# Kernel tuning notes

Measured on AMD Instinct MI355X. Metric: run time of the kernel, lower is better.

Reference implementation:

```python
import jax, jax.numpy as jnp
import numpy as np

DIMS = [1536, 2048, 2560, 3072, 1792, 2304, 2816, 2048, 2560, 3328]

def _ln(x, g, b, eps=1e-5):
    m = jnp.mean(x, -1, keepdims=True)
    v = jnp.mean((x - m) ** 2, -1, keepdims=True)
    return (x - m) / jnp.sqrt(v + eps) * g + b

def _gelu(x):
    return jax.nn.gelu(x, approximate=False)

def _mish(x):
    return x * jnp.tanh(jax.nn.softplus(x))

_ACTS = [jax.nn.silu, _gelu, _mish, jax.nn.relu, jax.nn.selu, jnp.tanh, jax.nn.softplus, jax.nn.elu]

def _renorm_sparse_topk(probs, active_k, max_k):
    vals, idx = jax.lax.top_k(probs, max_k)
    mask = (jnp.arange(max_k)[None, :] < active_k[:, None]).astype(probs.dtype)
    n = probs.shape[0]
    sparse = jnp.zeros_like(probs).at[jnp.arange(n)[:, None], idx].set(vals * mask)
    return sparse / jnp.clip(jnp.sum(sparse, -1, keepdims=True), 1e-6, None)

def setup_inputs():
    N, IN, OUT, E, M, S, SUB, DST, INNER, SH = 2048, 1024, 10, 10, 24, 4, 4, 40, 768, 2048
    DMAX = max(DIMS)
    ks = iter(jax.random.split(jax.random.key(0), 80))
    def p(shape, std=0.02):
        return jax.random.normal(next(ks), shape, jnp.float32) * std
    eu = np.zeros((E, DMAX, IN), np.float32)
    ed = np.zeros((E, OUT, DMAX), np.float32)
    for i in range(E):
        d = DIMS[i % len(DIMS)]
        eu[i, :d] = np.asarray(p((d, IN), 0.02))
        ed[i, :, :d] = np.asarray(p((OUT, d), 0.01))
    return {
        'x': jax.random.normal(next(ks), (N, IN), jnp.float32),
        'weight': p((OUT, IN), 0.03), 'bias': p((OUT,), 0.01),
        'shared_up_w': p((SH, IN)), 'shared_down_w': p((OUT, SH), 0.01),
        'shared_norm_g': jnp.ones((OUT,)), 'shared_norm_b': jnp.zeros((OUT,)),
        'shared_scale': jnp.asarray(1.0, jnp.float32),
        'memory_keys': p((M, IN)), 'memory_values_init': p((M, IN)),
        'memory_query_w': p((IN, IN), 0.01), 'memory_out_w': p((OUT, IN), 0.01),
        'mem_wgate_w': p((M, 2 * IN), 0.01), 'mem_wgate_b': jnp.zeros((M,)),
        'mem_wval_w': p((IN, IN), 0.01), 'mem_wval_b': jnp.zeros((IN,)),
        'depth_q_w': p((IN, IN), 0.01), 'depth_k_w': p((IN, IN), 0.01),
        'depth_v_w': p((IN, IN), 0.01), 'depth_out_w': p((OUT, IN), 0.01),
        'cell_ln_g': jnp.ones((S, IN)), 'cell_ln_b': jnp.zeros((S, IN)),
        'cell_fc1_w': p((S, INNER, IN)), 'cell_fc1_b': jnp.zeros((S, INNER)),
        'cell_fc2_w': p((S, IN, INNER)), 'cell_fc2_b': jnp.zeros((S, IN)),
        'ssm_a_w': p((DST, IN), 0.01), 'ssm_a_b': jnp.zeros((DST,)),
        'ssm_b_w': p((IN, DST), 0.01), 'ssm_b_b': jnp.zeros((IN,)),
        'mor_sub_w': p((SUB, E, IN)), 'mor_sub_b': jnp.zeros((SUB, E)),
        'mor_mix_w': p((SUB, IN)), 'mor_mix_b': jnp.zeros((SUB,)),
        'expert_bias': jnp.zeros((E,)),
        'budget_w': p((4, IN)), 'budget_b': jnp.zeros((4,)),
        'experts_up': jnp.asarray(eu), 'experts_down': jnp.asarray(ed),
        'expert_norm_g': jnp.ones((E, OUT)), 'expert_norm_b': jnp.zeros((E, OUT)),
        'halt_w': p((S, 1, IN), 0.01), 'halt_b': jnp.full((S, 1), -2.0, jnp.float32),
        'alpha': jnp.asarray(0.1, jnp.float32), 'beta': jnp.asarray(0.1, jnp.float32),
    }

def reference(x, weight, bias, shared_up_w, shared_down_w, shared_norm_g, shared_norm_b, shared_scale, memory_keys, memory_values_init, memory_query_w, memory_out_w, mem_wgate_w, mem_wgate_b, mem_wval_w, mem_wval_b, depth_q_w, depth_k_w, depth_v_w, depth_out_w, cell_ln_g, cell_ln_b, cell_fc1_w, cell_fc1_b, cell_fc2_w, cell_fc2_b, ssm_a_w, ssm_a_b, ssm_b_w, ssm_b_b, mor_sub_w, mor_sub_b, mor_mix_w, mor_mix_b, expert_bias, budget_w, budget_b, experts_up, experts_down, expert_norm_g, expert_norm_b, halt_w, halt_b, alpha, beta):
    in_dim = x.shape[-1]
    x_flat = x.reshape(-1, in_dim)
    n = x_flat.shape[0]
    base = x_flat @ weight.T + bias
    shared = _ln(jax.nn.silu(x_flat @ shared_up_w.T) @ shared_down_w.T, shared_norm_g, shared_norm_b)
    mem_vals = jnp.broadcast_to(memory_values_init[None], (n,) + memory_values_init.shape)
    current = x_flat
    total = jnp.zeros_like(base)
    cum_halt = jnp.zeros((n, 1), x.dtype)
    bank = []
    mem_scale = in_dim ** -0.5
    steps = cell_ln_g.shape[0]
    n_exp = expert_bias.shape[0]
    max_topk = min(4, n_exp)
    for step in range(steps):
        mq = current @ memory_query_w.T
        mem_attn = jax.nn.softmax((mq @ memory_keys.T) * mem_scale, -1)  # [n, M]
        mem_ctx = jnp.einsum('nm,nmd->nd', mem_attn, mem_vals)
        if bank:
            ds = jnp.stack(bank, 1)  # [n, s, d]
            q = current @ depth_q_w.T
            k = ds @ depth_k_w.T
            v = ds @ depth_v_w.T
            attn = jax.nn.softmax(jnp.einsum('nd,nsd->ns', q, k) * mem_scale, -1)
            depth_ctx = jnp.einsum('ns,nsd->nd', attn, v)
        else:
            depth_ctx = jnp.zeros_like(current)
        ssm_corr = jnp.tanh(current @ ssm_a_w.T + ssm_a_b) @ ssm_b_w.T + ssm_b_b
        enriched = current + 0.34 * mem_ctx + 0.22 * depth_ctx + 0.18 * ssm_corr
        h = _gelu(_ln(enriched, cell_ln_g[step], cell_ln_b[step]) @ cell_fc1_w[step].T + cell_fc1_b[step])
        current = enriched + h @ cell_fc2_w[step].T + cell_fc2_b[step]
        bank.append(current)
        sub = jnp.einsum('nd,sed->nse', current, mor_sub_w) + mor_sub_b[None]
        mix = jax.nn.softmax(current @ mor_mix_w.T + mor_mix_b, -1)
        gate_probs = jax.nn.softmax(jnp.einsum('ns,nse->ne', mix, sub) + expert_bias, -1)
        budget = 1 + jnp.argmax(jax.nn.softmax(current @ budget_w.T + budget_b, -1), -1)
        sg = _renorm_sparse_topk(gate_probs, budget, max_topk)
        expert_logits = jnp.zeros_like(base)
        for i in range(n_exp):
            d = DIMS[i % len(DIMS)]
            hh = _ACTS[i % len(_ACTS)](current @ experts_up[i, :d, :].T)
            eo = _ln(hh @ experts_down[i, :, :d].T, expert_norm_g[i], expert_norm_b[i])
            expert_logits = expert_logits + sg[:, i:i + 1] * eo
        step_logits = expert_logits + 0.22 * (mem_ctx @ memory_out_w.T) + 0.14 * (depth_ctx @ depth_out_w.T)
        surprise = 1.0 - jnp.max(sg, -1, keepdims=True)  # [n, 1]
        wg = jax.nn.softmax(jnp.concatenate([current, mem_ctx], -1) @ mem_wgate_w.T + mem_wgate_b, -1)
        wv = (current @ mem_wval_w.T + mem_wval_b)[:, None, :]
        mem_vals = mem_vals + surprise[..., None] * wg[..., None] * (wv - mem_vals)
        halt = jax.nn.sigmoid((current + 0.2 * mem_ctx + 0.1 * depth_ctx) @ halt_w[step].T + halt_b[step])
        remaining = 1.0 - cum_halt
        total = total + remaining * step_logits
        cum_halt = cum_halt + remaining * halt
    total = total / float(steps)
    out = base + shared_scale * shared + (alpha + 1e-4) * total + beta * (current @ memory_out_w.T)
    return out.reshape(x.shape[:-1] + (out.shape[-1],))
```

## Files before the change

kernel.cpp:

```cpp
#include <hip/hip_runtime.h>
#include <stdint.h>

#define N_TOK 2048
#define IN_D  1024
#define NEXP  10
#define NSTEP 4
#define INNER 768
#define SHD   2048
#define DMAX  3328
#define DSUM  24064

typedef __attribute__((ext_vector_type(4))) float f32x4;
typedef __attribute__((ext_vector_type(8))) short bf16x8;

__device__ const int c_dims[10] = {1536,2048,2560,3072,1792,2304,2816,2048,2560,3328};
__device__ const int c_offs[10] = {0,1536,3584,6144,9216,11008,13312,16128,18176,20736};
__device__ const int c_acts[10] = {0,1,2,3,4,5,6,7,0,1};
__device__ const int c_cum[11]  = {0,12,28,48,72,86,104,126,142,162,188};

__device__ __forceinline__ float wred(float v){
#pragma unroll
  for (int s = 32; s > 0; s >>= 1) v += __shfl_xor(v, s, 64);
  return v;
}
__device__ __forceinline__ float wmax(float v){
#pragma unroll
  for (int s = 32; s > 0; s >>= 1) v = fmaxf(v, __shfl_xor(v, s, 64));
  return v;
}
__device__ __forceinline__ float bf2f(uint16_t u){
  return __uint_as_float(((uint32_t)u) << 16);
}
__device__ __forceinline__ uint16_t f2bf(float f){
  uint32_t u = __float_as_uint(f);
  return (uint16_t)((u + 0x7FFFu + ((u >> 16) & 1u)) >> 16);
}
__device__ __forceinline__ uint8_t f2fp8(float f){
  uint32_t u = __float_as_uint(f);
  uint8_t sign = (uint8_t)((u >> 24) & 0x80u);
  uint32_t absu = u & 0x7FFFFFFFu;
  if (absu >= 0x43E00000u) return sign | 0x7Eu;
  if (absu < 0x3C800000u){
    float af = __uint_as_float(absu);
    int q = (int)rintf(af * 512.0f);
    return sign | (uint8_t)q;
  }
  uint32_t mant = absu & 0x7FFFFFu;
  uint32_t exp = absu >> 23;
  uint32_t lsb = (mant >> 20) & 1u;
  uint32_t rounded = mant + 0x7FFFFu + lsb;
  if (rounded >= 0x800000u){ exp += 1; rounded = 0; }
  uint32_t e8 = exp - 120;
  uint32_t m8 = (rounded >> 20) & 7u;
  if (e8 > 15u || (e8 == 15u && m8 == 7u)) return sign | 0x7Eu;
  return sign | (uint8_t)((e8 << 3) | m8);
}
__device__ __forceinline__ void gload16(const uint16_t* g, uint16_t* l){
  __builtin_amdgcn_global_load_lds(
      (const __attribute__((address_space(1))) uint32_t*)(const void*)g,
      (__attribute__((address_space(3))) uint32_t*)(void*)l, 16, 0, 0);
}
__device__ __forceinline__ void gload16b(const void* g, void* l){
  __builtin_amdgcn_global_load_lds(
      (const __attribute__((address_space(1))) uint32_t*)g,
      (__attribute__((address_space(3))) uint32_t*)l, 16, 0, 0);
}

__device__ __forceinline__ float actf(int a, float x){
  switch(a){
    case 0: return x / (1.f + expf(-x));
    case 1: return 0.5f * x * (1.f + erff(x * 0.7071067811865475f));
    case 2: { float sp = fmaxf(x,0.f) + log1pf(expf(-fabsf(x)));
              return x * tanhf(sp); }
    case 3: return fmaxf(x, 0.f);
    case 4: return x > 0.f ? 1.0507009873554805f * x
                           : 1.7580993408473768f * expm1f(x);
    case 5: return tanhf(x);
    case 6: return fmaxf(x,0.f) + log1pf(expf(-fabsf(x)));
    default: return x > 0.f ? x : expm1f(x);
  }
}

__global__ void split_kernel(const float* __restrict__ src, uint16_t* __restrict__ hi,
                             uint16_t* __restrict__ lo, size_t n){
  size_t i = ((size_t)blockIdx.x * blockDim.x + threadIdx.x) << 2;
  size_t stride = ((size_t)gridDim.x * blockDim.x) << 2;
  for (; i < n; i += stride){
    float4 v = *(const float4*)(src + i);
    ushort4 h, l;
    h.x = f2bf(v.x); l.x = f2bf(v.x - bf2f(h.x));
    h.y = f2bf(v.y); l.y = f2bf(v.y - bf2f(h.y));
    h.z = f2bf(v.z); l.z = f2bf(v.z - bf2f(h.z));
    h.w = f2bf(v.w); l.w = f2bf(v.w - bf2f(h.w));
    *(ushort4*)(hi + i) = h;
    *(ushort4*)(lo + i) = l;
  }
}
__global__ void split_strided(const float* __restrict__ src, uint16_t* __restrict__ hi,
                              uint16_t* __restrict__ lo, int rows, int cols, int ldd){
  int nq = rows * (cols >> 2);
  for (int i = blockIdx.x * blockDim.x + threadIdx.x; i < nq; i += gridDim.x * blockDim.x){
    int r = i / (cols >> 2), c4 = (i - r * (cols >> 2)) << 2;
    float4 v = *(const float4*)(src + (size_t)r * cols + c4);
    ushort4 h, l;
    h.x = f2bf(v.x); l.x = f2bf(v.x - bf2f(h.x));
    h.y = f2bf(v.y); l.y = f2bf(v.y - bf2f(h.y));
    h.z = f2bf(v.z); l.z = f2bf(v.z - bf2f(h.z));
    h.w = f2bf(v.w); l.w = f2bf(v.w - bf2f(h.w));
    size_t d = (size_t)r * ldd + c4;
    *(ushort4*)(hi + d) = h;
    *(ushort4*)(lo + d) = l;
  }
}
__global__ void cvt_fp8_kernel(const float* __restrict__ src, uint8_t* __restrict__ dst, size_t n){
  size_t i = ((size_t)blockIdx.x * blockDim.x + threadIdx.x) << 2;
  size_t stride = ((size_t)gridDim.x * blockDim.x) << 2;
  for (; i < n; i += stride){
    float4 v = *(const float4*)(src + i);
    uchar4 q;
    q.x = f2fp8(v.x); q.y = f2fp8(v.y); q.z = f2fp8(v.z); q.w = f2fp8(v.w);
    *(uchar4*)(dst + i) = q;
  }
}
__global__ void fill1_kernel(float* __restrict__ p, int n){
  int i = blockIdx.x * blockDim.x + threadIdx.x;
  if (i < n) p[i] = 1.f;
}
__global__ void tr_sbw_kernel(const float* __restrict__ src, float* __restrict__ dst){
  int i = blockIdx.x * 256 + threadIdx.x;
  if (i < 40 * 1024){
    int o = i >> 10, d = i & 1023;
    dst[i] = src[d * 40 + o];
  }
}

__global__ __launch_bounds__(256)
void k2_kernel(const float* __restrict__ keys, const float* __restrict__ mqw,
               float* __restrict__ K2){
  int m = blockIdx.x;
  int j = blockIdx.y * 256 + threadIdx.x;
  float acc = 0.f;
  for (int d = 0; d < 1024; d++)
    acc = fmaf(keys[m * 1024 + d], mqw[d * 1024 + j], acc);
  K2[m * 1024 + j] = acc;
}

__global__ void build_routew(const float* __restrict__ msw, const float* __restrict__ mmw,
                             const float* __restrict__ bw, const float* __restrict__ wgw,
                             const float* __restrict__ hw, const float* __restrict__ mow,
                             const float* __restrict__ dow, uint16_t* __restrict__ Wh,
                             uint16_t* __restrict__ Wl){
  const int TOT = 4 * 128 * 3072;
  for (int i = blockIdx.x * 256 + threadIdx.x; i < TOT; i += gridDim.x * 256){
    int t = i / (128 * 3072);
    int rem = i - t * (128 * 3072);
    int row = rem / 3072, col = rem - row * 3072;
    float v = 0.f;
    if (row < 40){ if (col < 1024) v = msw[row * 1024 + col]; }
    else if (row < 44){ if (col < 1024) v = mmw[(row - 40) * 1024 + col]; }
    else if (row < 48){ if (col < 1024) v = bw[(row - 44) * 1024 + col]; }
    else if (row < 72){ if (col < 2048) v = wgw[(row - 48) * 2048 + col]; }
    else if (row == 72){
      if (col < 1024) v = hw[t * 1024 + col];
      else if (col < 2048) v = 0.2f * hw[t * 1024 + col - 1024];
      else v = 0.1f * hw[t * 1024 + col - 2048];
    }
    else if (row < 83){ if (col >= 1024 && col < 2048) v = mow[(row - 73) * 1024 + col - 1024]; }
    else if (row < 93){ if (col >= 2048) v = dow[(row - 83) * 1024 + col - 2048]; }
    else if (row < 103){ if (col < 1024) v = mow[(row - 93) * 1024 + col]; }
    uint16_t h = f2bf(v);
    Wh[i] = h; Wl[i] = f2bf(v - bf2f(h));
  }
}

enum { EPI_GELU=0, EPI_CUR=1, EPI_PRE=2, EPI_QROUTE=3 };

template<int EPI>
__global__ __launch_bounds__(256)
void gemm_sp(const uint16_t* __restrict__ Ah, const uint16_t* __restrict__ Al, int lda,
             const uint16_t* __restrict__ Wh, const uint16_t* __restrict__ Wl,
             const uint16_t* __restrict__ W2h, const uint16_t* __restrict__ W2l,
             const float* __restrict__ bias, const float* __restrict__ addend,
             float* __restrict__ D0, float* __restrict__ D1, float* __restrict__ D2,
             float* __restrict__ D3, uint8_t* __restrict__ o8,
             uint16_t* __restrict__ oH, uint16_t* __restrict__ oL,
             int K, int D)
{
  __shared__ __align__(16) uint16_t sm[4][2][4096];
  int tid = threadIdx.x, lane = tid & 63, wave = tid >> 6;
  int wr = wave >> 1, wc = wave & 1;
  int arow = lane & 15, agrp = lane >> 4;
  int rowBase = blockIdx.y * 128;
  bool isRoute = (EPI == EPI_QROUTE) && ((int)blockIdx.x < 4);
  const uint16_t* Wsh = isRoute ? W2h : Wh;
  const uint16_t* Wsl = isRoute ? W2l : Wl;
  int wst     = isRoute ? 3072 : K;
  int colBase = isRoute ? 0 : ((EPI == EPI_QROUTE ? (int)blockIdx.x - 4 : (int)blockIdx.x) * 128);
  int kBase   = isRoute ? (int)blockIdx.x * 768 : 0;
  int kLen    = isRoute ? 768 : K;
  f32x4 acc[4][4];
#pragma unroll
  for (int m = 0; m < 4; m++)
#pragma unroll
    for (int n = 0; n < 4; n++){ f32x4 z = {0.f,0.f,0.f,0.f}; acc[m][n] = z; }

#define STAGE_G(buf, k0) do { \
  _Pragma("unroll") \
  for (int s = 0; s < 2; s++){ \
    int u = tid + s * 256; \
    int rr = u >> 2; \
    int ch = (u & 3) ^ ((rr >> 1) & 3); \
    size_t ga = (size_t)(rowBase + rr) * lda + kBase + (k0) + ch * 8; \
    size_t gw = (size_t)(colBase + rr) * wst + kBase + (k0) + ch * 8; \
    gload16(&Ah[ga], &sm[0][buf][u << 3]); \
    gload16(&Al[ga], &sm[1][buf][u << 3]); \
    gload16(&Wsh[gw], &sm[2][buf][u << 3]); \
    gload16(&Wsl[gw], &sm[3][buf][u << 3]); \
  } } while(0)

  int nk = kLen >> 5;
  STAGE_G(0, 0);
  if (nk > 1) STAGE_G(1, 32);
  int perm = (arow >> 1) & 3;
#pragma unroll 1
  for (int ki = 0; ki < nk; ki++){
    int cb = ki & 1;
    if (ki + 1 < nk) asm volatile("s_waitcnt vmcnt(8)" ::: "memory");
    else             asm volatile("s_waitcnt vmcnt(0)" ::: "memory");
    __builtin_amdgcn_s_barrier();
    bf16x8 ah[4], al[4], bh[4], bl[4];
#pragma unroll
    for (int m = 0; m < 4; m++){
      int u = ((wr*64 + m*16 + arow) << 2) + (agrp ^ perm);
      ah[m] = *(const bf16x8*)&sm[0][cb][u << 3];
      al[m] = *(const bf16x8*)&sm[1][cb][u << 3];
    }
#pragma unroll
    for (int n = 0; n < 4; n++){
      int u = ((wc*64 + n*16 + arow) << 2) + (agrp ^ perm);
      bh[n] = *(const bf16x8*)&sm[2][cb][u << 3];
      bl[n] = *(const bf16x8*)&sm[3][cb][u << 3];
    }
#pragma unroll
    for (int m = 0; m < 4; m++)
#pragma unroll
      for (int n = 0; n < 4; n++){
        acc[m][n] = __builtin_amdgcn_mfma_f32_16x16x32_bf16(ah[m], bh[n], acc[m][n], 0, 0, 0);
        acc[m][n] = __builtin_amdgcn_mfma_f32_16x16x32_bf16(ah[m], bl[n], acc[m][n], 0, 0, 0);
        acc[m][n] = __builtin_amdgcn_mfma_f32_16x16x32_bf16(al[m], bh[n], acc[m][n], 0, 0, 0);
      }
    __builtin_amdgcn_s_barrier();
    asm volatile("" ::: "memory");
    if (ki + 2 < nk) STAGE_G(cb, (ki + 2) << 5);
  }
#undef STAGE_G
#pragma unroll
  for (int m = 0; m < 4; m++){
#pragma unroll
    for (int n = 0; n < 4; n++){
      int col = colBase + wc*64 + n*16 + arow;
#pragma unroll
      for (int r2 = 0; r2 < 4; r2++){
        int row = rowBase + wr*64 + m*16 + agrp*4 + r2;
        float v = acc[m][n][r2];
        if (EPI == EPI_GELU){
          v += bias[col];
          v = 0.5f * v * (1.f + erff(v * 0.7071067811865475f));
          size_t idx = (size_t)row * D + col;
          uint16_t h = f2bf(v); oH[idx] = h; oL[idx] = f2bf(v - bf2f(h));
        }
        if (EPI == EPI_CUR){
          v += bias[col] + addend[(size_t)row * 1024 + col];
          D0[(size_t)row * 1024 + col] = v;
          size_t idx = (size_t)row * 3072 + col;
          uint16_t h = f2bf(v); oH[idx] = h; oL[idx] = f2bf(v - bf2f(h));
          o8[(size_t)row * 1024 + col] = f2fp8(v);
        }
        if (EPI == EPI_PRE){
          if (col < 2048) D0[(size_t)row * 2048 + col] = v / (1.f + expf(-v));
          else D1[(size_t)row * 128 + col - 2048] = v;
        }
        if (EPI == EPI_QROUTE){
          if (isRoute){
            D3[((size_t)blockIdx.x * N_TOK + row) * 128 + col] = v;
          } else {
            if (col < 1024) D0[(size_t)row * 1024 + col] = v;
            else if (col < 4096) D1[(size_t)row * 3072 + col - 1024] = v + bias[col - 1024];
            else if (col < 4160) D2[(size_t)row * 128 + col - 4096] = v;
          }
        }
      }
    }
  }
}

__global__ __launch_bounds__(256)
void expert_up_mfma(const uint8_t* __restrict__ A8, const uint8_t* __restrict__ U8,
                    const int* __restrict__ cnt, const int* __restrict__ gidx,
                    uint16_t* __restrict__ HH)
{
  int bid = blockIdx.x;
  int ex = bid / 192;
  int ey = bid - ex * 192;
  if (ey >= 188) return;
  int e = 0;
#pragma unroll
  for (int i = 1; i < 11; i++) if (ey >= c_cum[i]) e = i;
  int ct = ey - c_cum[e];
  int dcols = c_dims[e];
  int ne = cnt[e];
  const uint8_t* W = U8 + (size_t)e * DMAX * IN_D + (size_t)ct * 128 * IN_D;

  __shared__ __align__(16) uint8_t smem[32768];
  int tid = threadIdx.x, lane = tid & 63, wave = tid >> 6;
  int wr = wave >> 1, wc = wave & 1;
  int arow = lane & 15, agrp = lane >> 4;
  int actid = c_acts[e];
  size_t base_e = (size_t)N_TOK * c_offs[e];
  int rHalf = tid >> 1;
  int h16 = (((tid & 1) ^ ((tid >> 3) & 1)) << 4);
  int off = ((((agrp >> 1) ^ ((arow >> 2) & 1)) << 4) | ((agrp & 1) << 3));

#define STAGE_E(b, k0) do { \
    gload16b(&A8[(size_t)tok * IN_D + (k0) + h16], &smem[(b)*8192 + tid*16]); \
    gload16b(&W[(size_t)rHalf * IN_D + (k0) + h16], &smem[(b)*8192 + 4096 + tid*16]); \
  } while(0)

#pragma unroll 1
  for (int rowBase = ex * 128; rowBase < ne; rowBase += 4 * 128){
    int slot = rowBase + rHalf;
    int tok = (slot < ne) ? gidx[e * N_TOK + slot] : 0;

    f32x4 acc[4][4];
#pragma unroll
    for (int m = 0; m < 4; m++)
#pragma unroll
      for (int n = 0; n < 4; n++){ f32x4 z = {0.f,0.f,0.f,0.f}; acc[m][n] = z; }

    STAGE_E(0, 0);
    STAGE_E(1, 32);
    STAGE_E(2, 64);
    int cb = 0;
#pragma unroll 1
    for (int ki = 0; ki < 32; ki++){
      if (ki < 30)       asm volatile("s_waitcnt vmcnt(4)" ::: "memory");
      else if (ki == 30) asm volatile("s_waitcnt vmcnt(2)" ::: "memory");
      else               asm volatile("s_waitcnt vmcnt(0)" ::: "memory");
      __builtin_amdgcn_s_barrier();
      long a[4], b[4];
#pragma unroll
      for (int m = 0; m < 4; m++)
        a[m] = *(const long*)&smem[cb*8192 + (wr*64 + m*16 + arow)*32 + off];
#pragma unroll
      for (int n = 0; n < 4; n++)
        b[n] = *(const long*)&smem[cb*8192 + 4096 + (wc*64 + n*16 + arow)*32 + off];
#pragma unroll
      for (int m = 0; m < 4; m++)
#pragma unroll
        for (int n = 0; n < 4; n++)
          acc[m][n] = __builtin_amdgcn_mfma_f32_16x16x32_fp8_fp8(a[m], b[n], acc[m][n], 0, 0, 0);
      __builtin_amdgcn_s_barrier();
      asm volatile("" ::: "memory");
      if (ki + 3 < 32) STAGE_E(cb, (ki + 3) << 5);
      cb = (cb == 2) ? 0 : cb + 1;
    }
    uint16_t* Ht = (uint16_t*)smem;
#pragma unroll
    for (int m = 0; m < 4; m++){
      int rb0 = wr*64 + m*16 + agrp*4;
#pragma unroll
      for (int n = 0; n < 4; n++){
        int col = wc*64 + n*16 + arow;
#pragma unroll
        for (int r2 = 0; r2 < 4; r2++){
          int row = rb0 + r2;
          float v = actf(actid, acc[m][n][r2]);
          Ht[row * 128 + (col ^ ((row & 7) << 3))] = f2bf(v);
        }
      }
    }
    __syncthreads();
#pragma unroll
    for (int i = 0; i < 8; i++){
      int c = tid + i * 256;
      int row = c >> 4, chunk = c & 15;
      int schunk = (chunk & 8) | ((chunk ^ row) & 7);
      int4 val = *(const int4*)&Ht[row * 128 + schunk * 8];
      *(int4*)&HH[base_e + (size_t)(rowBase + row) * dcols
                  + (size_t)ct * 128 + chunk * 8] = val;
    }
    __syncthreads();
  }
#undef STAGE_E
}

__global__ __launch_bounds__(256)
void ctx_enr_kernel(const float* __restrict__ qaux, const float* __restrict__ dqbuf,
                    const float* __restrict__ Ac, const float* __restrict__ W0,
                    const float* __restrict__ W1, const float* __restrict__ W2,
                    const float* __restrict__ mvi,
                    const float* __restrict__ t0, const float* __restrict__ t1,
                    const float* __restrict__ t2, const float* __restrict__ cur,
                    const float* __restrict__ sab, const float* __restrict__ sbwT,
                    const float* __restrict__ sbb, const float* __restrict__ lng,
                    const float* __restrict__ lnbv,
                    float* __restrict__ enr, uint16_t* __restrict__ lnh,
                    uint16_t* __restrict__ lnl, uint16_t* __restrict__ Arh,
                    uint16_t* __restrict__ Arl, int t)
{
  int row0 = blockIdx.x * 4;
  int tid = threadIdx.x, lane = tid & 63, wave = tid >> 6;
  int roww = row0 + wave;
  __shared__ float su[4][24], ss[4][3], de[4][3], s40[4][40], redm[4][8];
  __shared__ float sev[4][1024];
  {
    float pj = (lane < 24) ? qaux[(size_t)roww * 128 + lane] * 0.03125f : -1e30f;
    float mx = wmax(pj);
    float ex = (lane < 24) ? expf(pj - mx) : 0.f;
    float sum = wred(ex);
    float attn = ex / sum;
    if (lane < 24) su[wave][lane] = attn * Ac[roww * 24 + lane];
    float w0v = (t > 0 && lane < 24) ? W0[roww * 24 + lane] : 0.f;
    float s0 = wred(attn * w0v);
    float w1v = (t > 1 && lane < 24) ? W1[roww * 24 + lane] : 0.f;
    float s1 = wred(attn * w1v);
    float w2v = (t > 2 && lane < 24) ? W2[roww * 24 + lane] : 0.f;
    float s2 = wred(attn * w2v);
    if (lane == 0){ ss[wave][0] = s0; ss[wave][1] = s1; ss[wave][2] = s2; }
    if (lane < 40) s40[wave][lane] = tanhf(qaux[(size_t)roww * 128 + 24 + lane] + sab[lane]);
  }
  if (t > 0){
    size_t tbw = (size_t)roww * 3072;
    float a0 = 0.f, a1 = 0.f, a2 = 0.f;
    for (int d = lane; d < 1024; d += 64){
      float dq = dqbuf[(size_t)roww * 1024 + d];
      a0 = fmaf(dq, t0[tbw + d], a0);
      if (t > 1) a1 = fmaf(dq, t1[tbw + d], a1);
      if (t > 2) a2 = fmaf(dq, t2[tbw + d], a2);
    }
    a0 = wred(a0) * 0.03125f; a1 = wred(a1) * 0.03125f; a2 = wred(a2) * 0.03125f;
    float dmx = a0;
    if (t > 1) dmx = fmaxf(dmx, a1);
    if (t > 2) dmx = fmaxf(dmx, a2);
    float e0 = expf(a0 - dmx);
    float e1 = (t > 1) ? expf(a1 - dmx) : 0.f;
    float e2 = (t > 2) ? expf(a2 - dmx) : 0.f;
    float dinv = 1.f / (e0 + e1 + e2);
    if (lane == 0){ de[wave][0] = e0 * dinv; de[wave][1] = e1 * dinv; de[wave][2] = e2 * dinv; }
  } else if (lane == 0){ de[wave][0] = 0.f; de[wave][1] = 0.f; de[wave][2] = 0.f; }
  __syncthreads();
  float part0 = 0.f, part1 = 0.f, part2 = 0.f, part3 = 0.f;
#pragma unroll 1
  for (int j = 0; j < 4; j++){
    int d = tid + j * 256;
    float mv[4] = {0.f,0.f,0.f,0.f};
    float sv[4] = {0.f,0.f,0.f,0.f};
#pragma unroll 8
    for (int m = 0; m < 24; m++){
      float w = mvi[m * 1024 + d];
#pragma unroll
      for (int r = 0; r < 4; r++) mv[r] = fmaf(su[r][m], w, mv[r]);
    }
#pragma unroll 8
    for (int o = 0; o < 40; o++){
      float w = sbwT[o * 1024 + d];
#pragma unroll
      for (int r = 0; r < 4; r++) sv[r] = fmaf(s40[r][o], w, sv[r]);
    }
    float sbbv = sbb[d];
#pragma unroll
    for (int r = 0; r < 4; r++){
      int row = row0 + r;
      size_t tb = (size_t)row * 3072;
      float mvr = mv[r], dvr = 0.f;
      if (t > 0){
        mvr = fmaf(ss[r][0], t0[tb + 2048 + d], mvr);
        dvr = de[r][0] * t0[tb + 1024 + d];
        if (t > 1){ mvr = fmaf(ss[r][1], t1[tb + 2048 + d], mvr); dvr = fmaf(de[r][1], t1[tb + 1024 + d], dvr); }
        if (t > 2){ mvr = fmaf(ss[r][2], t2[tb + 2048 + d], mvr); dvr = fmaf(de[r][2], t2[tb + 1024 + d], dvr); }
      }
      float v = cur[(size_t)row * 1024 + d] + 0.34f * mvr + 0.22f * dvr
              + 0.18f * (sbbv + sv[r]);
      size_t ar = (size_t)row * 3072;
      uint16_t mh = f2bf(mvr);
      Arh[ar + 1024 + d] = mh; Arl[ar + 1024 + d] = f2bf(mvr - bf2f(mh));
      uint16_t dh = f2bf(dvr);
      Arh[ar + 2048 + d] = dh; Arl[ar + 2048 + d] = f2bf(dvr - bf2f(dh));
      sev[r][d] = v;
      if (r == 0) part0 += v; else if (r == 1) part1 += v;
      else if (r == 2) part2 += v; else part3 += v;
    }
  }
  {
    float p0 = wred(part0), p1 = wred(part1), p2 = wred(part2), p3 = wred(part3);
    if (lane == 0){ redm[0][wave] = p0; redm[1][wave] = p1; redm[2][wave] = p2; redm[3][wave] = p3; }
  }
  __syncthreads();
  float mean0 = (redm[0][0]+redm[0][1]+redm[0][2]+redm[0][3]) * (1.f/1024.f);
  float mean1 = (redm[1][0]+redm[1][1]+redm[1][2]+redm[1][3]) * (1.f/1024.f);
  float mean2 = (redm[2][0]+redm[2][1]+redm[2][2]+redm[2][3]) * (1.f/1024.f);
  float mean3 = (redm[3][0]+redm[3][1]+redm[3][2]+redm[3][3]) * (1.f/1024.f);
  float vp0 = 0.f, vp1 = 0.f, vp2 = 0.f, vp3 = 0.f;
#pragma unroll
  for (int j = 0; j < 4; j++){
    int d = tid + j * 256;
    float d0 = sev[0][d] - mean0; vp0 = fmaf(d0, d0, vp0);
    float d1 = sev[1][d] - mean1; vp1 = fmaf(d1, d1, vp1);
    float d2 = sev[2][d] - mean2; vp2 = fmaf(d2, d2, vp2);
    float d3 = sev[3][d] - mean3; vp3 = fmaf(d3, d3, vp3);
  }
  {
    float p0 = wred(vp0), p1 = wred(vp1), p2 = wred(vp2), p3 = wred(vp3);
    if (lane == 0){ redm[0][4+wave] = p0; redm[1][4+wave] = p1; redm[2][4+wave] = p2; redm[3][4+wave] = p3; }
  }
  __syncthreads();
  float rs0 = 1.f / sqrtf((redm[0][4]+redm[0][5]+redm[0][6]+redm[0][7]) * (1.f/1024.f) + 1e-5f);
  float rs1 = 1.f / sqrtf((redm[1][4]+redm[1][5]+redm[1][6]+redm[1][7]) * (1.f/1024.f) + 1e-5f);
  float rs2 = 1.f / sqrtf((redm[2][4]+redm[2][5]+redm[2][6]+redm[2][7]) * (1.f/1024.f) + 1e-5f);
  float rs3 = 1.f / sqrtf((redm[3][4]+redm[3][5]+redm[3][6]+redm[3][7]) * (1.f/1024.f) + 1e-5f);
#pragma unroll 1
  for (int j = 0; j < 4; j++){
    int d = tid + j * 256;
    float lg = lng[t * 1024 + d], lb = lnbv[t * 1024 + d];
    float mean[4] = {mean0, mean1, mean2, mean3};
    float rs[4] = {rs0, rs1, rs2, rs3};
#pragma unroll
    for (int r = 0; r < 4; r++){
      int row = row0 + r;
      size_t idx = (size_t)row * 1024 + d;
      float v0 = sev[r][d];
      enr[idx] = v0;
      float v = (v0 - mean[r]) * rs[r] * lg + lb;
      uint16_t h = f2bf(v);
      lnh[idx] = h;
      lnl[idx] = f2bf(v - bf2f(h));
    }
  }
}

__global__ __launch_bounds__(256)
void route_fin(const float* __restrict__ ROq, const float* __restrict__ mmb,
               const float* __restrict__ msb, const float* __restrict__ ebias,
               const float* __restrict__ bb, const float* __restrict__ wgb,
               const float* __restrict__ hb,
               float* __restrict__ sg, float* __restrict__ haltb,
               float* __restrict__ Ac, float* __restrict__ W0,
               float* __restrict__ W1, float* __restrict__ W2,
               int* __restrict__ cnt, int* __restrict__ gidx,
               int* __restrict__ pos, float* __restrict__ routeS, int t)
{
  int row = blockIdx.x * 256 + threadIdx.x;
  int lane = threadIdx.x & 63;
  const size_t P = (size_t)N_TOK * 128;
  const float* r0 = ROq + (size_t)row * 128;
  const float* r1 = r0 + P;
  const float* r2 = r0 + 2 * P;
  const float* r3 = r0 + 3 * P;
  auto R = [&](int j){ return r0[j] + r1[j] + r2[j] + r3[j]; };
  float pm[4];
#pragma unroll
  for (int o = 0; o < 4; o++) pm[o] = R(40 + o) + mmb[o];
  float mmx = fmaxf(fmaxf(pm[0], pm[1]), fmaxf(pm[2], pm[3]));
  float msum = 0.f;
#pragma unroll
  for (int o = 0; o < 4; o++){ pm[o] = expf(pm[o] - mmx); msum += pm[o]; }
  float minv = 1.f / msum;
  float gl[10];
#pragma unroll
  for (int e = 0; e < 10; e++){
    float g = ebias[e];
#pragma unroll
    for (int s2 = 0; s2 < 4; s2++)
      g = fmaf(pm[s2] * minv, R(s2 * 10 + e) + msb[s2 * 10 + e], g);
    gl[e] = g;
  }
  float gmx = gl[0];
#pragma unroll
  for (int e = 1; e < 10; e++) gmx = fmaxf(gmx, gl[e]);
  float gs = 0.f;
#pragma unroll
  for (int e = 0; e < 10; e++){ gl[e] = expf(gl[e] - gmx); gs += gl[e]; }
  float ginv = 1.f / gs;
#pragma unroll
  for (int e = 0; e < 10; e++) gl[e] *= ginv;
  float pb0 = R(44) + bb[0], pb1 = R(45) + bb[1], pb2 = R(46) + bb[2], pb3 = R(47) + bb[3];
  int bud = 1; float bbest = pb0;
  if (pb1 > bbest){ bbest = pb1; bud = 2; }
  if (pb2 > bbest){ bbest = pb2; bud = 3; }
  if (pb3 > bbest){ bbest = pb3; bud = 4; }
  float tv[4]; int ti[4]; unsigned used = 0;
#pragma unroll
  for (int j = 0; j < 4; j++){
    float best = -1e30f; int bi = 0;
#pragma unroll
    for (int e = 0; e < 10; e++){
      bool ok = (!((used >> e) & 1u)) && (gl[e] > best);
      if (ok){ best = gl[e]; bi = e; }
    }
    tv[j] = best; ti[j] = bi; used |= (1u << bi);
  }
  float ssum = tv[0];
  if (bud > 1) ssum += tv[1];
  if (bud > 2) ssum += tv[2];
  if (bud > 3) ssum += tv[3];
  float den = fmaxf(ssum, 1e-6f);
  float sup = 1.f - tv[0] / den;
  float sgv[10];
#pragma unroll
  for (int e = 0; e < 10; e++){
    float sv = 0.f;
#pragma unroll
    for (int j = 0; j < 4; j++) if (j < bud && ti[j] == e) sv = tv[j] / den;
    sgv[e] = sv;
    sg[row * 10 + e] = sv;
  }
  float pw[24];
#pragma unroll
  for (int m = 0; m < 24; m++) pw[m] = R(48 + m) + wgb[m];
  float wmx2 = pw[0];
#pragma unroll
  for (int m = 1; m < 24; m++) wmx2 = fmaxf(wmx2, pw[m]);
  float wsum = 0.f;
#pragma unroll
  for (int m = 0; m < 24; m++){ pw[m] = expf(pw[m] - wmx2); wsum += pw[m]; }
  float winv = 1.f / wsum;
#pragma unroll
  for (int m = 0; m < 24; m++){
    float c = sup * pw[m] * winv;
    float om = 1.f - c;
    Ac[row * 24 + m] *= om;
    if (t > 0) W0[row * 24 + m] *= om;
    if (t > 1) W1[row * 24 + m] *= om;
    if (t > 2) W2[row * 24 + m] *= om;
    if (t == 0)      W0[row * 24 + m] = c;
    else if (t == 1) W1[row * 24 + m] = c;
    else if (t == 2) W2[row * 24 + m] = c;
  }
  haltb[row] = 1.f / (1.f + expf(-(R(72) + hb[t])));
#pragma unroll
  for (int i = 0; i < 30; i++) routeS[row * 32 + i] = R(73 + i);
#pragma unroll
  for (int e = 0; e < 10; e++){
    bool act = sgv[e] != 0.f;
    unsigned long long mask = __ballot(act);
    int cw = __popcll(mask);
    int b0 = 0;
    if (lane == 0 && cw > 0) b0 = atomicAdd(&cnt[e], cw);
    b0 = __shfl(b0, 0, 64);
    if (act){
      int slot = b0 + __popcll(mask & ((1ull << lane) - 1ull));
      gidx[e * N_TOK + slot] = row;
      pos[row * 10 + e] = slot;
    }
  }
}

__global__ __launch_bounds__(256)
void downfin_kernel(const uint16_t* __restrict__ HH, const int* __restrict__ pos,
                    const float* __restrict__ ED, const float* __restrict__ sg,
                    const float* __restrict__ eng, const float* __restrict__ enb,
                    const float* __restrict__ routeS, const float* __restrict__ haltb,
                    float* __restrict__ total, float* __restrict__ cumh)
{
  int lane = threadIdx.x & 63;
  int row = blockIdx.x * 4 + (threadIdx.x >> 6);
  float out[10] = {};
  for (int e = 0; e < NEXP; e++){
    float g = sg[row * 10 + e];
    if (g != 0.0f){
      int d = c_dims[e];
      int slot = pos[row * 10 + e];
      const uint16_t* hr = HH + (size_t)N_TOK * c_offs[e] + (size_t)slot * d;
      const float* wd = ED + (size_t)e * 10 * DMAX;
      float p[10] = {};
      for (int k = lane * 4; k < d; k += 256){
        uint2 hv = *(const uint2*)&hr[k];
        float h0 = bf2f((uint16_t)hv.x), h1 = bf2f((uint16_t)(hv.x >> 16));
        float h2 = bf2f((uint16_t)hv.y), h3 = bf2f((uint16_t)(hv.y >> 16));
#pragma unroll
        for (int o = 0; o < 10; o++){
          float4 w4 = *(const float4*)&wd[o * DMAX + k];
          p[o] = fmaf(h0, w4.x, fmaf(h1, w4.y, fmaf(h2, w4.z, fmaf(h3, w4.w, p[o]))));
        }
      }
#pragma unroll
      for (int o = 0; o < 10; o++) p[o] = wred(p[o]);
      float mean = 0.f;
#pragma unroll
      for (int o = 0; o < 10; o++) mean += p[o];
      mean *= 0.1f;
      float var = 0.f;
#pragma unroll
      for (int o = 0; o < 10; o++){ float dd = p[o] - mean; var += dd * dd; }
      var *= 0.1f;
      float rs = 1.f / sqrtf(var + 1e-5f);
#pragma unroll
      for (int o = 0; o < 10; o++)
        out[o] += g * ((p[o] - mean) * rs * eng[e * 10 + o] + enb[e * 10 + o]);
    }
  }
  if (lane == 0){
    const float* r = routeS + (size_t)row * 32;
    float rem = 1.f - cumh[row];
#pragma unroll
    for (int o = 0; o < 10; o++)
      total[row * 10 + o] += rem * (out[o] + 0.22f * r[o] + 0.14f * r[10 + o]);
    cumh[row] += rem * haltb[row];
  }
}

__global__ __launch_bounds__(256)
void shared_kernel(const float* __restrict__ shpre, const float* __restrict__ sdw,
                   const float* __restrict__ g, const float* __restrict__ b,
                   float* __restrict__ outp)
{
  int lane = threadIdx.x & 63;
  int row = blockIdx.x * 4 + (threadIdx.x >> 6);
  const float* xr = shpre + (size_t)row * SHD;
  float p[10];
#pragma unroll
  for (int o = 0; o < 10; o++) p[o] = 0.f;
  for (int k = lane; k < SHD; k += 64){
    float xv = xr[k];
#pragma unroll
    for (int o = 0; o < 10; o++) p[o] = fmaf(xv, sdw[o * SHD + k], p[o]);
  }
#pragma unroll
  for (int o = 0; o < 10; o++) p[o] = wred(p[o]);
  float mean = 0.f;
#pragma unroll
  for (int o = 0; o < 10; o++) mean += p[o];
  mean *= 0.1f;
  float var = 0.f;
#pragma unroll
  for (int o = 0; o < 10; o++){ float dd = p[o] - mean; var += dd * dd; }
  var *= 0.1f;
  float rs = 1.f / sqrtf(var + 1e-5f);
  if (lane == 0){
#pragma unroll
    for (int o = 0; o < 10; o++) outp[row * 10 + o] = (p[o] - mean) * rs * g[o] + b[o];
  }
}

__global__ __launch_bounds__(256)
void final_lite(const float* __restrict__ qaux, const float* __restrict__ biasp,
                const float* __restrict__ sharedp, const float* __restrict__ total,
                const float* __restrict__ routeS, const float* __restrict__ sscale,
                const float* __restrict__ alphap, const float* __restrict__ betap,
                float* __restrict__ outp)
{
  int row = blockIdx.x * 256 + threadIdx.x;
  float ss = sscale[0], av = alphap[0] + 1e-4f, bv = betap[0];
#pragma unroll
  for (int o = 0; o < 10; o++)
    outp[row * 10 + o] = (qaux[(size_t)row * 128 + 64 + o] + biasp[o])
                       + ss * sharedp[row * 10 + o]
                       + av * (total[row * 10 + o] * 0.25f)
                       + bv * routeS[(size_t)row * 32 + 20 + o];
}

extern "C" void kernel_launch(void* const* d_in, const int* in_sizes, int n_in,
                              void* d_out, int out_size, void* d_ws, size_t ws_size,
                              hipStream_t stream)
{
  const float* x     = (const float*)d_in[0];
  const float* wgt   = (const float*)d_in[1];
  const float* bias  = (const float*)d_in[2];
  const float* suw   = (const float*)d_in[3];
  const float* sdw   = (const float*)d_in[4];
  const float* sng   = (const float*)d_in[5];
  const float* snb   = (const float*)d_in[6];
  const float* sscale= (const float*)d_in[7];
  const float* keys  = (const float*)d_in[8];
  const float* mvi   = (const float*)d_in[9];
  const float* mqw   = (const float*)d_in[10];
  const float* mow   = (const float*)d_in[11];
  const float* wgw   = (const float*)d_in[12];
  const float* wgb   = (const float*)d_in[13];
  const float* wvw   = (const float*)d_in[14];
  const float* wvb   = (const float*)d_in[15];
  const float* dqw   = (const float*)d_in[16];
  const float* dkw   = (const float*)d_in[17];
  const float* dvw   = (const float*)d_in[18];
  const float* dow   = (const float*)d_in[19];
  const float* clng  = (const float*)d_in[20];
  const float* clnb  = (const float*)d_in[21];
  const float* fc1w  = (const float*)d_in[22];
  const float* fc1b  = (const float*)d_in[23];
  const float* fc2w  = (const float*)d_in[24];
  const float* fc2b  = (const float*)d_in[25];
  const float* saw   = (const float*)d_in[26];
  const float* sab   = (const float*)d_in[27];
  const float* sbw   = (const float*)d_in[28];
  const float* sbb   = (const float*)d_in[29];
  const float* msw   = (const float*)d_in[30];
  const float* msb   = (const float*)d_in[31];
  const float* mmw   = (const float*)d_in[32];
  const float* mmb   = (const float*)d_in[33];
  const float* ebias = (const float*)d_in[34];
  const float* bw    = (const float*)d_in[35];
  const float* bb    = (const float*)d_in[36];
  const float* eup   = (const float*)d_in[37];
  const float* edn   = (const float*)d_in[38];
  const float* eng   = (const float*)d_in[39];
  const float* enb   = (const float*)d_in[40];
  const float* hw    = (const float*)d_in[41];
  const float* hb    = (const float*)d_in[42];
  const float* alphap= (const float*)d_in[43];
  const float* betap = (const float*)d_in[44];
  float* outp = (float*)d_out;

  char* wsb = (char*)d_ws;
  size_t off = 0;
  auto AL = [&](size_t bytes) -> void* {
    void* p = wsb + off;
    off = (off + bytes + 255) & ~(size_t)255;
    return p;
  };
  const size_t NI = (size_t)N_TOK * IN_D;
  float* cur    = (float*)AL(NI * 4);
  float* enr    = (float*)AL(NI * 4);
  float* dqbuf  = (float*)AL(NI * 4);
  float* qaux   = (float*)AL((size_t)N_TOK * 128 * 4);
  float* routeQ = (float*)AL((size_t)4 * N_TOK * 128 * 4);
  float* routeS = (float*)AL((size_t)N_TOK * 32 * 4);
  float* trio0  = (float*)AL((size_t)N_TOK * 3072 * 4);
  float* trio1  = (float*)AL((size_t)N_TOK * 3072 * 4);
  float* trio2  = (float*)AL((size_t)N_TOK * 3072 * 4);
  float* Ac     = (float*)AL((size_t)N_TOK * 24 * 4);
  float* W0     = (float*)AL((size_t)N_TOK * 24 * 4);
  float* W1     = (float*)AL((size_t)N_TOK * 24 * 4);
  float* W2     = (float*)AL((size_t)N_TOK * 24 * 4);
  float* sg     = (float*)AL((size_t)N_TOK * 10 * 4);
  float* haltb  = (float*)AL((size_t)N_TOK * 4);
  char*  zblk   = (char*)AL((size_t)N_TOK * 10 * 4 + N_TOK * 4 + 4 * 16 * 4);
  float* total  = (float*)zblk;
  float* cumh   = (float*)(zblk + (size_t)N_TOK * 10 * 4);
  int*   cnt    = (int*)(zblk + (size_t)N_TOK * 10 * 4 + N_TOK * 4);
  int*   gidx   = (int*)AL((size_t)NEXP * N_TOK * 4);
  int*   pos    = (int*)AL((size_t)N_TOK * NEXP * 4);
  float* sharedp= (float*)AL((size_t)N_TOK * 10 * 4);
  float* cbias  = (float*)AL(3072 * 4);
  float* K2f    = (float*)AL((size_t)24 * 1024 * 4);
  float* sbwT   = (float*)AL((size_t)40 * 1024 * 4);
  uint16_t* lnh  = (uint16_t*)AL(NI * 2);
  uint16_t* lnl  = (uint16_t*)AL(NI * 2);
  uint16_t* h7h  = (uint16_t*)AL((size_t)N_TOK * INNER * 2);
  uint16_t* h7l  = (uint16_t*)AL((size_t)N_TOK * INNER * 2);
  uint16_t* Arh  = (uint16_t*)AL((size_t)N_TOK * 3072 * 2);
  uint16_t* Arl  = (uint16_t*)AL((size_t)N_TOK * 3072 * 2);
  const size_t W1M = (size_t)IN_D * IN_D;
  uint16_t* preWh  = (uint16_t*)AL((size_t)2176 * 1024 * 2);
  uint16_t* preWl  = (uint16_t*)AL((size_t)2176 * 1024 * 2);
  uint16_t* qtWh   = (uint16_t*)AL((size_t)4224 * 1024 * 2);
  uint16_t* qtWl   = (uint16_t*)AL((size_t)4224 * 1024 * 2);
  uint16_t* rtWh   = (uint16_t*)AL((size_t)4 * 128 * 3072 * 2);
  uint16_t* rtWl   = (uint16_t*)AL((size_t)4 * 128 * 3072 * 2);
  const size_t WFC = (size_t)NSTEP * INNER * IN_D;
  uint16_t* fc1wh = (uint16_t*)AL(WFC * 2); uint16_t* fc1wl = (uint16_t*)AL(WFC * 2);
  uint16_t* fc2wh = (uint16_t*)AL(WFC * 2); uint16_t* fc2wl = (uint16_t*)AL(WFC * 2);
  uint8_t* upbf8 = (uint8_t*)AL((size_t)NEXP * DMAX * IN_D);
  uint8_t* A8    = (uint8_t*)AL(NI);
  uint16_t* HHc  = (uint16_t*)AL((size_t)N_TOK * DSUM * 2);
  float* shpre  = (float*)HHc;

  hipMemsetAsync(zblk, 0, (size_t)N_TOK * 10 * 4 + N_TOK * 4 + 4 * 16 * 4, stream);
  hipMemsetAsync(cbias, 0, 3072 * 4, stream);
  hipMemcpyAsync(cbias + 2048, wvb, 1024 * 4, hipMemcpyDeviceToDevice, stream);
  hipMemcpyAsync(cur, x, NI * 4, hipMemcpyDeviceToDevice, stream);
  fill1_kernel<<<(N_TOK * 24 + 255) / 256, 256, 0, stream>>>(Ac, N_TOK * 24);
  cvt_fp8_kernel<<<2048, 256, 0, stream>>>(eup, upbf8, (size_t)NEXP * DMAX * IN_D);
  tr_sbw_kernel<<<160, 256, 0, stream>>>(sbw, sbwT);

  split_strided<<<1024, 256, 0, stream>>>(x, Arh, Arl, N_TOK, 1024, 3072);
  split_kernel<<<1024, 256, 0, stream>>>(suw, preWh, preWl, (size_t)SHD * 1024);
  split_kernel<<<256, 256, 0, stream>>>(saw, preWh + (size_t)2072*1024, preWl + (size_t)2072*1024, (size_t)40 * 1024);
  split_kernel<<<256, 256, 0, stream>>>(wgt, preWh + (size_t)2112*1024, preWl + (size_t)2112*1024, (size_t)10 * 1024);
  hipMemsetAsync(preWh + (size_t)2122*1024, 0, (size_t)54 * 1024 * 2, stream);
  hipMemsetAsync(preWl + (size_t)2122*1024, 0, (size_t)54 * 1024 * 2, stream);
  split_kernel<<<1024, 256, 0, stream>>>(dqw, qtWh, qtWl, W1M);
  split_kernel<<<1024, 256, 0, stream>>>(dkw, qtWh + W1M, qtWl + W1M, W1M);
  split_kernel<<<1024, 256, 0, stream>>>(dvw, qtWh + 2*W1M, qtWl + 2*W1M, W1M);
  split_kernel<<<1024, 256, 0, stream>>>(wvw, qtWh + 3*W1M, qtWl + 3*W1M, W1M);
  split_kernel<<<256, 256, 0, stream>>>(saw, qtWh + (size_t)4120*1024, qtWl + (size_t)4120*1024, (size_t)40 * 1024);
  hipMemsetAsync(qtWh + (size_t)4160*1024, 0, (size_t)64 * 1024 * 2, stream);
  hipMemsetAsync(qtWl + (size_t)4160*1024, 0, (size_t)64 * 1024 * 2, stream);
  k2_kernel<<<dim3(24, 4), 256, 0, stream>>>(keys, mqw, K2f);
  split_kernel<<<256, 256, 0, stream>>>(K2f, preWh + (size_t)2048*1024, preWl + (size_t)2048*1024, (size_t)24 * 1024);
  split_kernel<<<256, 256, 0, stream>>>(K2f, qtWh + (size_t)4096*1024, qtWl + (size_t)4096*1024, (size_t)24 * 1024);
  build_routew<<<2048, 256, 0, stream>>>(msw, mmw, bw, wgw, hw, mow, dow, rtWh, rtWl);
  split_kernel<<<1024, 256, 0, stream>>>(fc1w, fc1wh, fc1wl, WFC);
  split_kernel<<<1024, 256, 0, stream>>>(fc2w, fc2wh, fc2wl, WFC);

  gemm_sp<EPI_PRE><<<dim3(17, 16), 256, 0, stream>>>(
      Arh, Arl, 3072, preWh, preWl, nullptr, nullptr, nullptr, nullptr,
      shpre, qaux, nullptr, nullptr, nullptr, nullptr, nullptr, IN_D, 2176);
  shared_kernel<<<512, 256, 0, stream>>>(shpre, sdw, sng, snb, sharedp);

  float* trioB[3] = {trio0, trio1, trio2};

  for (int t = 0; t < NSTEP; t++){
    ctx_enr_kernel<<<512, 256, 0, stream>>>(qaux, dqbuf, Ac, W0, W1, W2, mvi,
                                            trio0, trio1, trio2, cur, sab, sbwT, sbb,
                                            clng, clnb, enr, lnh, lnl, Arh, Arl, t);
    gemm_sp<EPI_GELU><<<dim3(INNER/128, 16), 256, 0, stream>>>(
        lnh, lnl, 1024, fc1wh + (size_t)t * INNER * IN_D, fc1wl + (size_t)t * INNER * IN_D,
        nullptr, nullptr, fc1b + t * INNER, nullptr,
        nullptr, nullptr, nullptr, nullptr, nullptr, h7h, h7l, IN_D, INNER);
    gemm_sp<EPI_CUR><<<dim3(8, 16), 256, 0, stream>>>(
        h7h, h7l, 768, fc2wh + (size_t)t * IN_D * INNER, fc2wl + (size_t)t * IN_D * INNER,
        nullptr, nullptr, fc2b + t * IN_D, enr,
        cur, nullptr, nullptr, nullptr, A8, Arh, Arl, INNER, IN_D);
    gemm_sp<EPI_QROUTE><<<dim3(t < 3 ? 37 : 4, 16), 256, 0, stream>>>(
        Arh, Arl, 3072, qtWh, qtWl,
        rtWh + (size_t)t * 128 * 3072, rtWl + (size_t)t * 128 * 3072,
        cbias, nullptr, dqbuf, t < 3 ? trioB[t] : nullptr, qaux, routeQ,
        nullptr, nullptr, nullptr, IN_D, 4224);
    route_fin<<<8, 256, 0, stream>>>(routeQ, mmb, msb, ebias, bb, wgb, hb,
                                     sg, haltb, Ac, W0, W1, W2,
                                     cnt + t * 16, gidx, pos, routeS, t);
    expert_up_mfma<<<768, 256, 0, stream>>>(A8, upbf8, cnt + t * 16, gidx, HHc);
    downfin_kernel<<<512, 256, 0, stream>>>(HHc, pos, edn, sg, eng, enb,
                                            routeS, haltb, total, cumh);
  }
  final_lite<<<8, 256, 0, stream>>>(qaux, bias, sharedp, total, routeS,
                                    sscale, alphap, betap, outp);
}
```

Baseline: 1.783 ms.

## Fuse expert down-projection into expert up GEMM epilogue with atomic partial sums

The expert-up MFMA kernel now multiplies its activated 128-column hidden tile by the matching slice of the down-projection weights in its epilogue, then atomically adds 10-wide partial logits per token and expert into a small buffer. This removes the large bf16 hidden-activation buffer write and the separate down-projection read pass in downfin, which becomes a tiny per-token LayerNorm and accumulate kernel. route_fin zeroes the partial buffer for selected experts. The cost is float atomics, which make summation order nondeterministic, plus extra shared-memory weight staging and epilogue FMA work.

```diff
diff --git a/kernel.cpp b/kernel.cpp
--- a/kernel.cpp
+++ b/kernel.cpp
@@ -297,7 +297,7 @@
 __global__ __launch_bounds__(256)
 void expert_up_mfma(const uint8_t* __restrict__ A8, const uint8_t* __restrict__ U8,
                     const int* __restrict__ cnt, const int* __restrict__ gidx,
-                    uint16_t* __restrict__ HH)
+                    const float* __restrict__ ED, float* __restrict__ EL2)
 {
   int bid = blockIdx.x;
   int ex = bid / 192;
@@ -307,19 +307,24 @@
 #pragma unroll
   for (int i = 1; i < 11; i++) if (ey >= c_cum[i]) e = i;
   int ct = ey - c_cum[e];
-  int dcols = c_dims[e];
   int ne = cnt[e];
   const uint8_t* W = U8 + (size_t)e * DMAX * IN_D + (size_t)ct * 128 * IN_D;
 
   __shared__ __align__(16) uint8_t smem[32768];
+  __shared__ float swd[1280];
   int tid = threadIdx.x, lane = tid & 63, wave = tid >> 6;
   int wr = wave >> 1, wc = wave & 1;
   int arow = lane & 15, agrp = lane >> 4;
   int actid = c_acts[e];
-  size_t base_e = (size_t)N_TOK * c_offs[e];
   int rHalf = tid >> 1;
   int h16 = (((tid & 1) ^ ((tid >> 3) & 1)) << 4);
   int off = ((((agrp >> 1) ^ ((arow >> 2) & 1)) << 4) | ((agrp & 1) << 3));
+
+#pragma unroll
+  for (int i = tid; i < 1280; i += 256){
+    int o = i >> 7, col = i & 127;
+    swd[i] = ED[((size_t)e * 10 + o) * DMAX + ct * 128 + col];
+  }
 
 #define STAGE_E(b, k0) do { \
     gload16b(&A8[(size_t)tok * IN_D + (k0) + h16], &smem[(b)*8192 + tid*16]); \
@@ -380,14 +385,32 @@
       }
     }
     __syncthreads();
-#pragma unroll
-    for (int i = 0; i < 8; i++){
-      int c = tid + i * 256;
-      int row = c >> 4, chunk = c & 15;
-      int schunk = (chunk & 8) | ((chunk ^ row) & 7);
-      int4 val = *(const int4*)&Ht[row * 128 + schunk * 8];
-      *(int4*)&HH[base_e + (size_t)(rowBase + row) * dcols
-                  + (size_t)ct * 128 + chunk * 8] = val;
+    {
+      int drow = tid >> 1, half = tid & 1;
+      int grow = rowBase + drow;
+      float p[10] = {0.f,0.f,0.f,0.f,0.f,0.f,0.f,0.f,0.f,0.f};
+      const uint32_t* Ht32 = (const uint32_t*)Ht;
+      int swzr = (drow & 7) << 2;
+      if (grow < ne){
+#pragma unroll 8
+        for (int j = 0; j < 32; j++){
+          int cp = half * 32 + j;
+          uint32_t h2 = Ht32[drow * 64 + (cp ^ swzr)];
+          float h0 = bf2f((uint16_t)h2), h1 = bf2f((uint16_t)(h2 >> 16));
+          int c2 = cp * 2;
+#pragma unroll
+          for (int o = 0; o < 10; o++)
+            p[o] = fmaf(h0, swd[o*128 + c2], fmaf(h1, swd[o*128 + c2 + 1], p[o]));
+        }
+      }
+#pragma unroll
+      for (int o = 0; o < 10; o++){
+        float v = p[o] + __shfl_xor(p[o], 1, 64);
+        if (half == 0 && grow < ne){
+          int tokd = gidx[e * N_TOK + grow];
+          atomicAdd(&EL2[((size_t)tokd * 10 + e) * 10 + o], v);
+        }
+      }
     }
     __syncthreads();
   }
@@ -547,7 +570,7 @@
                float* __restrict__ Ac, float* __restrict__ W0,
                float* __restrict__ W1, float* __restrict__ W2,
                int* __restrict__ cnt, int* __restrict__ gidx,
-               int* __restrict__ pos, float* __restrict__ routeS, int t)
+               float* __restrict__ EL2, float* __restrict__ routeS, int t)
 {
   int row = blockIdx.x * 256 + threadIdx.x;
   int lane = threadIdx.x & 63;
@@ -613,6 +636,10 @@
     for (int j = 0; j < 4; j++) if (j < bud && ti[j] == e) sv = tv[j] / den;
     sgv[e] = sv;
     sg[row * 10 + e] = sv;
+    if (sv != 0.f){
+#pragma unroll
+      for (int o = 0; o < 10; o++) EL2[((size_t)row * 10 + e) * 10 + o] = 0.f;
+    }
   }
   float pw[24];
 #pragma unroll
@@ -650,63 +677,43 @@
     if (act){
       int slot = b0 + __popcll(mask & ((1ull << lane) - 1ull));
       gidx[e * N_TOK + slot] = row;
-      pos[row * 10 + e] = slot;
     }
   }
 }
 
 __global__ __launch_bounds__(256)
-void downfin_kernel(const uint16_t* __restrict__ HH, const int* __restrict__ pos,
-                    const float* __restrict__ ED, const float* __restrict__ sg,
+void downfin_kernel(const float* __restrict__ EL2, const float* __restrict__ sg,
                     const float* __restrict__ eng, const float* __restrict__ enb,
                     const float* __restrict__ routeS, const float* __restrict__ haltb,
                     float* __restrict__ total, float* __restrict__ cumh)
 {
-  int lane = threadIdx.x & 63;
-  int row = blockIdx.x * 4 + (threadIdx.x >> 6);
+  int row = blockIdx.x * 256 + threadIdx.x;
   float out[10] = {};
   for (int e = 0; e < NEXP; e++){
     float g = sg[row * 10 + e];
     if (g != 0.0f){
-      int d = c_dims[e];
-      int slot = pos[row * 10 + e];
-      const uint16_t* hr = HH + (size_t)N_TOK * c_offs[e] + (size_t)slot * d;
-      const float* wd = ED + (size_t)e * 10 * DMAX;
-      float p[10] = {};
-      for (int k = lane * 4; k < d; k += 256){
-        uint2 hv = *(const uint2*)&hr[k];
-        float h0 = bf2f((uint16_t)hv.x), h1 = bf2f((uint16_t)(hv.x >> 16));
-        float h2 = bf2f((uint16_t)hv.y), h3 = bf2f((uint16_t)(hv.y >> 16));
-#pragma unroll
-        for (int o = 0; o < 10; o++){
-          float4 w4 = *(const float4*)&wd[o * DMAX + k];
-          p[o] = fmaf(h0, w4.x, fmaf(h1, w4.y, fmaf(h2, w4.z, fmaf(h3, w4.w, p[o]))));
-        }
-      }
-#pragma unroll
-      for (int o = 0; o < 10; o++) p[o] = wred(p[o]);
+      const float* p = &EL2[((size_t)row * 10 + e) * 10];
+      float pv[10];
       float mean = 0.f;
 #pragma unroll
-      for (int o = 0; o < 10; o++) mean += p[o];
+      for (int o = 0; o < 10; o++){ pv[o] = p[o]; mean += pv[o]; }
       mean *= 0.1f;
       float var = 0.f;
 #pragma unroll
-      for (int o = 0; o < 10; o++){ float dd = p[o] - mean; var += dd * dd; }
+      for (int o = 0; o < 10; o++){ float dd = pv[o] - mean; var += dd * dd; }
       var *= 0.1f;
       float rs = 1.f / sqrtf(var + 1e-5f);
 #pragma unroll
       for (int o = 0; o < 10; o++)
-        out[o] += g * ((p[o] - mean) * rs * eng[e * 10 + o] + enb[e * 10 + o]);
-    }
-  }
-  if (lane == 0){
-    const float* r = routeS + (size_t)row * 32;
-    float rem = 1.f - cumh[row];
-#pragma unroll
-    for (int o = 0; o < 10; o++)
-      total[row * 10 + o] += rem * (out[o] + 0.22f * r[o] + 0.14f * r[10 + o]);
-    cumh[row] += rem * haltb[row];
-  }
+        out[o] += g * ((pv[o] - mean) * rs * eng[e * 10 + o] + enb[e * 10 + o]);
+    }
+  }
+  const float* r = routeS + (size_t)row * 32;
+  float rem = 1.f - cumh[row];
+#pragma unroll
+  for (int o = 0; o < 10; o++)
+    total[row * 10 + o] += rem * (out[o] + 0.22f * r[o] + 0.14f * r[10 + o]);
+  cumh[row] += rem * haltb[row];
 }
 
 __global__ __launch_bounds__(256)
@@ -838,7 +845,7 @@
   float* cumh   = (float*)(zblk + (size_t)N_TOK * 10 * 4);
   int*   cnt    = (int*)(zblk + (size_t)N_TOK * 10 * 4 + N_TOK * 4);
   int*   gidx   = (int*)AL((size_t)NEXP * N_TOK * 4);
-  int*   pos    = (int*)AL((size_t)N_TOK * NEXP * 4);
+  float* EL2    = (float*)AL((size_t)N_TOK * 100 * 4);
   float* sharedp= (float*)AL((size_t)N_TOK * 10 * 4);
   float* cbias  = (float*)AL(3072 * 4);
   float* K2f    = (float*)AL((size_t)24 * 1024 * 4);
@@ -861,8 +868,7 @@
   uint16_t* fc2wh = (uint16_t*)AL(WFC * 2); uint16_t* fc2wl = (uint16_t*)AL(WFC * 2);
   uint8_t* upbf8 = (uint8_t*)AL((size_t)NEXP * DMAX * IN_D);
   uint8_t* A8    = (uint8_t*)AL(NI);
-  uint16_t* HHc  = (uint16_t*)AL((size_t)N_TOK * DSUM * 2);
-  float* shpre  = (float*)HHc;
+  float* shpre   = (float*)AL((size_t)N_TOK * SHD * 4);
 
   hipMemsetAsync(zblk, 0, (size_t)N_TOK * 10 * 4 + N_TOK * 4 + 4 * 16 * 4, stream);
   hipMemsetAsync(cbias, 0, 3072 * 4, stream);
@@ -918,10 +924,10 @@
         nullptr, nullptr, nullptr, IN_D, 4224);
     route_fin<<<8, 256, 0, stream>>>(routeQ, mmb, msb, ebias, bb, wgb, hb,
                                      sg, haltb, Ac, W0, W1, W2,
-                                     cnt + t * 16, gidx, pos, routeS, t);
-    expert_up_mfma<<<768, 256, 0, stream>>>(A8, upbf8, cnt + t * 16, gidx, HHc);
-    downfin_kernel<<<512, 256, 0, stream>>>(HHc, pos, edn, sg, eng, enb,
-                                            routeS, haltb, total, cumh);
+                                     cnt + t * 16, gidx, EL2, routeS, t);
+    expert_up_mfma<<<768, 256, 0, stream>>>(A8, upbf8, cnt + t * 16, gidx, edn, EL2);
+    downfin_kernel<<<8, 256, 0, stream>>>(EL2, sg, eng, enb,
+                                          routeS, haltb, total, cumh);
   }
   final_lite<<<8, 256, 0, stream>>>(qaux, bias, sharedp, total, routeS,
                                     sscale, alphap, betap, outp);
```

New measurement: 1.927 ms. 8.1% more time.
